# Kernel tuning notes

Hardware: AMD Instinct MI355X
Metric: run time of the kernel (lower is better)

## Reference

```python
import jax, jax.numpy as jnp
import numpy as np

B, S, HID, NH, HD, INTER, NB = 4, 4096, 2048, 32, 64, 8192, 8
EPS = 1e-5
MEM_EPS = 1e-6


def rmsnorm(x, w, eps=EPS):
    return x * jax.lax.rsqrt(jnp.mean(x * x, axis=-1, keepdims=True) + eps) * w


def hbit_linear(x, w):
    # BitNet b1.58: ternary weights (absmean scale) + int8 per-token activation quant (STE).
    ws = jnp.mean(jnp.abs(w)) + 1e-8
    wq = jnp.round(jnp.clip(w / ws, -1.0, 1.0)) * ws
    w_eff = w + jax.lax.stop_gradient(wq - w)
    xs = 127.0 / jnp.clip(jnp.max(jnp.abs(x), axis=-1, keepdims=True), 1e-5, None)
    xq = jnp.clip(jnp.round(x * xs), -128.0, 127.0) / xs
    x_eff = x + jax.lax.stop_gradient(xq - x)
    return x_eff @ w_eff.T


def infini_attention(xn, wq, wk, wv, wo, beta):
    # xn: [B,S,HID]; segment-wise causal local attention + compressive linear memory.
    def proj(w):
        return (xn @ w.T).reshape(B, S, NH, HD).transpose(0, 2, 1, 3)  # [B,H,S,D]

    q, k, v = proj(wq), proj(wk), proj(wv)
    seg = S // NB

    def to_segs(t):
        return t.reshape(B, NH, NB, seg, HD).transpose(2, 0, 1, 3, 4)  # [NB,B,H,seg,D]

    qs, ks, vs = to_segs(q), to_segs(k), to_segs(v)
    mask = jnp.tril(jnp.ones((seg, seg), bool))
    g = jax.nn.sigmoid(beta)[None, :, None, None]  # per-head memory/local mix
    scale = 1.0 / np.sqrt(HD)

    def step(carry, inp):
        M, z = carry  # M:[B,H,D,D], z:[B,H,D]
        qc, kc, vc = inp
        sq = jax.nn.elu(qc) + 1.0
        sk = jax.nn.elu(kc) + 1.0
        a_mem = jnp.einsum('bhsd,bhde->bhse', sq, M) / (
            jnp.einsum('bhsd,bhd->bhs', sq, z)[..., None] + MEM_EPS)
        scores = jnp.einsum('bhqd,bhkd->bhqk', qc, kc) * scale
        scores = jnp.where(mask, scores, -1e9)
        a_loc = jnp.einsum('bhqk,bhkd->bhqd', jax.nn.softmax(scores, axis=-1), vc)
        M = M + jnp.einsum('bhsd,bhse->bhde', sk, vc)
        z = z + sk.sum(axis=2)
        out = g * a_mem + (1.0 - g) * a_loc
        return (M, z), out

    M0 = jnp.zeros((B, NH, HD, HD), xn.dtype)
    z0 = jnp.zeros((B, NH, HD), xn.dtype)
    _, outs = jax.lax.scan(step, (M0, z0), (qs, ks, vs))  # [NB,B,H,seg,D]
    out = outs.transpose(1, 2, 0, 3, 4).reshape(B, NH, S, HD)
    out = out.transpose(0, 2, 1, 3).reshape(B, S, HID)
    return out @ wo.T


def setup_inputs() -> dict:
    key = jax.random.key(0)
    ks = jax.random.split(key, 12)
    std = 0.02
    return {
        'x': jax.random.normal(ks[0], (B, S, HID), jnp.float32),
        'wq': jax.random.normal(ks[1], (HID, HID), jnp.float32) * std,
        'wk': jax.random.normal(ks[2], (HID, HID), jnp.float32) * std,
        'wv': jax.random.normal(ks[3], (HID, HID), jnp.float32) * std,
        'wo': jax.random.normal(ks[4], (HID, HID), jnp.float32) * std,
        'beta': jnp.zeros((NH,), jnp.float32),
        'gate': jnp.zeros((1,), jnp.float32),
        'attn_norm_w': jnp.ones((HID,), jnp.float32),
        'mlp_norm_w': jnp.ones((HID,), jnp.float32),
        'attn_res_norm_w': jnp.ones((HID,), jnp.float32),
        'attn_res_scale': jnp.full((1,), 0.1, jnp.float32),
        'mlp_res_norm_w': jnp.ones((HID,), jnp.float32),
        'mlp_res_scale': jnp.full((1,), 0.1, jnp.float32),
        'ffn_up_w': jax.random.normal(ks[5], (2 * INTER, HID), jnp.float32) * std,
        'ffn_down_w': jax.random.normal(ks[6], (HID, INTER), jnp.float32) * std,
    }


def reference(x, wq, wk, wv, wo, beta, gate, attn_norm_w, mlp_norm_w,
              attn_res_norm_w, attn_res_scale, mlp_res_norm_w, mlp_res_scale,
              ffn_up_w, ffn_down_w):
    residual = x
    xn = rmsnorm(x, attn_norm_w)
    infini_out = infini_attention(xn, wq, wk, wv, wo, beta)
    gated = jax.nn.sigmoid(gate) * infini_out
    x = residual + attn_res_scale * rmsnorm(gated, attn_res_norm_w)
    residual = x
    xn = rmsnorm(x, mlp_norm_w)
    up = hbit_linear(xn, ffn_up_w)
    gate_up, value = jnp.split(up, 2, axis=-1)
    mlp_out = hbit_linear(jax.nn.silu(gate_up) * value, ffn_down_w)
    x = residual + mlp_res_scale * rmsnorm(mlp_out, mlp_res_norm_w)
    return x
```

## Files before the change

kernel.cpp:

```cpp
#include <hip/hip_runtime.h>
#include <cstdint>
#include <cstddef>

typedef unsigned int u32;
typedef unsigned short u16;
typedef __bf16 bf16x8 __attribute__((ext_vector_type(8)));
typedef float f32x4 __attribute__((ext_vector_type(4)));
typedef float f32x16 __attribute__((ext_vector_type(16)));
typedef int i32x4 __attribute__((ext_vector_type(4)));

#define DEV static __device__ __forceinline__

DEV float bf2f(u16 u) { u32 x = ((u32)u) << 16; return __builtin_bit_cast(float, x); }
DEV u16 f2bf(float f) {
  u32 u = __builtin_bit_cast(u32, f);
  u32 r = (u + 0x7fffu + ((u >> 16) & 1u)) >> 16;
  return (u16)r;
}
DEV u32 pkbf(float a, float b) {
  __bf16 ba = (__bf16)a, bb = (__bf16)b;
  return (u32)__builtin_bit_cast(u16, ba) | ((u32)__builtin_bit_cast(u16, bb) << 16);
}
DEV u32 pk4i8(float a, float b, float c, float d) {
  return (u32)(unsigned char)(char)a | ((u32)(unsigned char)(char)b << 8) |
         ((u32)(unsigned char)(char)c << 16) | ((u32)(unsigned char)(char)d << 24);
}
DEV void bf8tof(const uint4 v, float* f) {
  f[0] = bf2f((u16)(v.x & 0xffffu)); f[1] = bf2f((u16)(v.x >> 16));
  f[2] = bf2f((u16)(v.y & 0xffffu)); f[3] = bf2f((u16)(v.y >> 16));
  f[4] = bf2f((u16)(v.z & 0xffffu)); f[5] = bf2f((u16)(v.z >> 16));
  f[6] = bf2f((u16)(v.w & 0xffffu)); f[7] = bf2f((u16)(v.w >> 16));
}
DEV uint4 f8tobf(const float* f) {
  uint4 r;
  r.x = (u32)f2bf(f[0]) | ((u32)f2bf(f[1]) << 16);
  r.y = (u32)f2bf(f[2]) | ((u32)f2bf(f[3]) << 16);
  r.z = (u32)f2bf(f[4]) | ((u32)f2bf(f[5]) << 16);
  r.w = (u32)f2bf(f[6]) | ((u32)f2bf(f[7]) << 16);
  return r;
}
DEV float sigmoidf_(float x) { return 1.f / (1.f + expf(-x)); }

DEV float wred_sum(float v) {
  #pragma unroll
  for (int m = 32; m; m >>= 1) v += __shfl_xor(v, m, 64);
  return v;
}
DEV float wred_max(float v) {
  #pragma unroll
  for (int m = 32; m; m >>= 1) v = fmaxf(v, __shfl_xor(v, m, 64));
  return v;
}
DEV float block_sum(float v, float* red, int nw) {
  v = wred_sum(v);
  int w = threadIdx.x >> 6, l = threadIdx.x & 63;
  if (l == 0) red[w] = v;
  __syncthreads();
  float t = red[0];
  for (int i = 1; i < nw; ++i) t += red[i];
  __syncthreads();
  return t;
}
DEV float block_max(float v, float* red, int nw) {
  v = wred_max(v);
  int w = threadIdx.x >> 6, l = threadIdx.x & 63;
  if (l == 0) red[w] = v;
  __syncthreads();
  float t = red[0];
  for (int i = 1; i < nw; ++i) t = fmaxf(t, red[i]);
  __syncthreads();
  return t;
}
DEV void gload16(const void* g, void* l) {
  __builtin_amdgcn_global_load_lds((const __attribute__((address_space(1))) void*)g,
                                   (__attribute__((address_space(3))) void*)l, 16, 0, 0);
}
DEV bf16x8 ldfrag(const u16* p) {
  uint4 u = *(const uint4*)p;
  return __builtin_bit_cast(bf16x8, u);
}

#define BN_ 4
#define S_ 4096
#define HID_ 2048
#define NH_ 32
#define HD_ 64
#define INTER_ 8192
#define NBSEG_ 8
#define SEG_ 512
#define TOK_ 16384
#define CHROWS_ 4096
#define LDQ_ 6144

__global__ __launch_bounds__(256) void castf2b(const float* __restrict__ a, u16* __restrict__ o) {
  size_t idx = ((size_t)blockIdx.x * 256 + threadIdx.x) * 4;
  float4 v = *(const float4*)(a + idx);
  float f[4] = {v.x, v.y, v.z, v.w};
  uint2 r;
  r.x = (u32)f2bf(f[0]) | ((u32)f2bf(f[1]) << 16);
  r.y = (u32)f2bf(f[2]) | ((u32)f2bf(f[3]) << 16);
  *(uint2*)(o + idx) = r;
}

__global__ __launch_bounds__(256) void absmean_part(const float* __restrict__ w, float* __restrict__ part) {
  __shared__ float red[4];
  size_t base = (size_t)blockIdx.x * 16384 + threadIdx.x * 4;
  float s = 0.f;
  #pragma unroll
  for (int i = 0; i < 16; ++i) {
    float4 v = *(const float4*)(w + base + (size_t)i * 1024);
    s += fabsf(v.x) + fabsf(v.y) + fabsf(v.z) + fabsf(v.w);
  }
  float t = block_sum(s, red, 4);
  if (threadIdx.x == 0) part[blockIdx.x] = t;
}

__global__ __launch_bounds__(256) void absmean_fin(const float* __restrict__ part, int n, float invN, float* __restrict__ outp) {
  __shared__ float red[4];
  float s = 0.f;
  for (int i = threadIdx.x; i < n; i += 256) s += part[i];
  float t = block_sum(s, red, 4);
  if (threadIdx.x == 0) outp[0] = t * invN + 1e-8f;
}

__global__ __launch_bounds__(256) void ternarize_i8(const float* __restrict__ w, const float* __restrict__ wsp, char* __restrict__ o) {
  size_t idx = ((size_t)blockIdx.x * 256 + threadIdx.x) * 4;
  const float inv = 1.f / wsp[0];
  float4 v = *(const float4*)(w + idx);
  float q0 = rintf(fminf(fmaxf(v.x * inv, -1.f), 1.f));
  float q1 = rintf(fminf(fmaxf(v.y * inv, -1.f), 1.f));
  float q2 = rintf(fminf(fmaxf(v.z * inv, -1.f), 1.f));
  float q3 = rintf(fminf(fmaxf(v.w * inv, -1.f), 1.f));
  *(u32*)(o + idx) = pk4i8(q0, q1, q2, q3);
}

__global__ __launch_bounds__(256) void rmsnorm_cast(const float* __restrict__ x, const float* __restrict__ wn, u16* __restrict__ o) {
  __shared__ float red[4];
  const int r = blockIdx.x, tid = threadIdx.x;
  const float* xr = x + (size_t)r * HID_;
  float vx[8];
  #pragma unroll
  for (int i = 0; i < 2; ++i) {
    float4 t = *(const float4*)(xr + tid * 8 + i * 4);
    vx[i * 4 + 0] = t.x; vx[i * 4 + 1] = t.y; vx[i * 4 + 2] = t.z; vx[i * 4 + 3] = t.w;
  }
  float ss = 0.f;
  #pragma unroll
  for (int j = 0; j < 8; ++j) ss += vx[j] * vx[j];
  float tot = block_sum(ss, red, 4);
  float rstd = rsqrtf(tot * (1.f / HID_) + 1e-5f);
  float wv[8];
  #pragma unroll
  for (int i = 0; i < 2; ++i) {
    float4 t = *(const float4*)(wn + tid * 8 + i * 4);
    wv[i * 4 + 0] = t.x; wv[i * 4 + 1] = t.y; wv[i * 4 + 2] = t.z; wv[i * 4 + 3] = t.w;
  }
  float ov[8];
  #pragma unroll
  for (int j = 0; j < 8; ++j) ov[j] = vx[j] * rstd * wv[j];
  *(uint4*)(o + (size_t)r * HID_ + tid * 8) = f8tobf(ov);
}

__global__ __launch_bounds__(256) void resid1_rms2(const float* __restrict__ x, const u16* __restrict__ ao,
    const float* __restrict__ gatep, const float* __restrict__ w1, const float* __restrict__ rsp,
    const float* __restrict__ w2, float* __restrict__ x2, char* __restrict__ xq, float* __restrict__ xs1) {
  __shared__ float red[4];
  const int r = blockIdx.x, tid = threadIdx.x;
  const float g = sigmoidf_(gatep[0]);
  const float rs = rsp[0];
  uint4 av = *(const uint4*)(ao + (size_t)r * HID_ + tid * 8);
  float f[8]; bf8tof(av, f);
  float ss = 0.f;
  #pragma unroll
  for (int j = 0; j < 8; ++j) { f[j] *= g; ss += f[j] * f[j]; }
  float tot = block_sum(ss, red, 4);
  float rstd1 = rsqrtf(tot * (1.f / HID_) + 1e-5f);
  const float* xr = x + (size_t)r * HID_;
  float xv2[8];
  #pragma unroll
  for (int i = 0; i < 2; ++i) {
    float4 xv = *(const float4*)(xr + tid * 8 + i * 4);
    float4 wv = *(const float4*)(w1 + tid * 8 + i * 4);
    xv2[i * 4 + 0] = xv.x + rs * f[i * 4 + 0] * rstd1 * wv.x;
    xv2[i * 4 + 1] = xv.y + rs * f[i * 4 + 1] * rstd1 * wv.y;
    xv2[i * 4 + 2] = xv.z + rs * f[i * 4 + 2] * rstd1 * wv.z;
    xv2[i * 4 + 3] = xv.w + rs * f[i * 4 + 3] * rstd1 * wv.w;
  }
  float* o = x2 + (size_t)r * HID_;
  *(float4*)(o + tid * 8) = float4{xv2[0], xv2[1], xv2[2], xv2[3]};
  *(float4*)(o + tid * 8 + 4) = float4{xv2[4], xv2[5], xv2[6], xv2[7]};
  float ss2 = 0.f;
  #pragma unroll
  for (int j = 0; j < 8; ++j) ss2 += xv2[j] * xv2[j];
  float tot2 = block_sum(ss2, red, 4);
  float rstd2 = rsqrtf(tot2 * (1.f / HID_) + 1e-5f);
  float xn[8]; float mx = 0.f;
  #pragma unroll
  for (int i = 0; i < 2; ++i) {
    float4 wv = *(const float4*)(w2 + tid * 8 + i * 4);
    xn[i * 4 + 0] = xv2[i * 4 + 0] * rstd2 * wv.x;
    xn[i * 4 + 1] = xv2[i * 4 + 1] * rstd2 * wv.y;
    xn[i * 4 + 2] = xv2[i * 4 + 2] * rstd2 * wv.z;
    xn[i * 4 + 3] = xv2[i * 4 + 3] * rstd2 * wv.w;
  }
  #pragma unroll
  for (int j = 0; j < 8; ++j) mx = fmaxf(mx, fabsf(xn[j]));
  float bm = block_max(mx, red, 4);
  float xs = 127.f / fmaxf(bm, 1e-5f);
  float q[8];
  #pragma unroll
  for (int j = 0; j < 8; ++j) q[j] = fminf(fmaxf(rintf(xn[j] * xs), -128.f), 127.f);
  uint2 pw;
  pw.x = pk4i8(q[0], q[1], q[2], q[3]);
  pw.y = pk4i8(q[4], q[5], q[6], q[7]);
  *(uint2*)(xq + (size_t)r * HID_ + tid * 8) = pw;
  if (tid == 0) xs1[r] = xs;
}

__global__ __launch_bounds__(256) void quant_h_i8(const u16* __restrict__ hb, char* __restrict__ hq, float* __restrict__ xs2) {
  __shared__ float red[4];
  const int r = blockIdx.x, tid = threadIdx.x;
  const u16* hr = hb + (size_t)r * INTER_ + tid * 32;
  float f[32];
  #pragma unroll
  for (int k = 0; k < 4; ++k) {
    uint4 v = *(const uint4*)(hr + k * 8);
    bf8tof(v, &f[k * 8]);
  }
  float mx = 0.f;
  #pragma unroll
  for (int j = 0; j < 32; ++j) mx = fmaxf(mx, fabsf(f[j]));
  float bm = block_max(mx, red, 4);
  float xs = 127.f / fmaxf(bm, 1e-5f);
  u32 pw[8];
  #pragma unroll
  for (int k = 0; k < 8; ++k) {
    float q[4];
    #pragma unroll
    for (int j = 0; j < 4; ++j) q[j] = fminf(fmaxf(rintf(f[k * 4 + j] * xs), -128.f), 127.f);
    pw[k] = pk4i8(q[0], q[1], q[2], q[3]);
  }
  char* oq = hq + (size_t)r * INTER_ + tid * 32;
  *(uint4*)oq = uint4{pw[0], pw[1], pw[2], pw[3]};
  *(uint4*)(oq + 16) = uint4{pw[4], pw[5], pw[6], pw[7]};
  if (tid == 0) xs2[r] = xs;
}

__global__ __launch_bounds__(256) void final_resid(const float* __restrict__ x2, const u16* __restrict__ mlp,
    const float* __restrict__ wn, const float* __restrict__ rsp, float* __restrict__ out) {
  __shared__ float red[4];
  const int r = blockIdx.x, tid = threadIdx.x;
  const float rs = rsp[0];
  uint4 mv = *(const uint4*)(mlp + (size_t)r * HID_ + tid * 8);
  float f[8]; bf8tof(mv, f);
  float ss = 0.f;
  #pragma unroll
  for (int j = 0; j < 8; ++j) ss += f[j] * f[j];
  float tot = block_sum(ss, red, 4);
  float rstd = rsqrtf(tot * (1.f / HID_) + 1e-5f);
  const float* xr = x2 + (size_t)r * HID_;
  float* o = out + (size_t)r * HID_;
  #pragma unroll
  for (int i = 0; i < 2; ++i) {
    float4 xv = *(const float4*)(xr + tid * 8 + i * 4);
    float4 wv = *(const float4*)(wn + tid * 8 + i * 4);
    float4 ov;
    ov.x = xv.x + rs * f[i * 4 + 0] * rstd * wv.x;
    ov.y = xv.y + rs * f[i * 4 + 1] * rstd * wv.y;
    ov.z = xv.z + rs * f[i * 4 + 2] * rstd * wv.z;
    ov.w = xv.w + rs * f[i * 4 + 3] * rstd * wv.w;
    *(float4*)(o + tid * 8 + i * 4) = ov;
  }
}

template<int NBN>
__global__ __launch_bounds__(512, 2)
void gemm_bt2(const u16* __restrict__ A, const u16* __restrict__ Bw, u16* __restrict__ C,
              int K, int ldc) {
  __shared__ __align__(16) u16 As[128 * 64];
  __shared__ __align__(16) u16 Bs[256 * 64];
  const int tid = threadIdx.x;
  const int w = tid >> 6, lane = tid & 63;
  const int l15 = lane & 15, l4 = lane >> 4;
  const int wr = (w >> 2) * 64, wc = (w & 3) * 64;
  int id = blockIdx.x;
  const int cpx = (int)gridDim.x >> 3;
  id = (id & 7) * cpx + (id >> 3);
  const int bm = id / NBN, bn = id % NBN;
  const u16* Ag = A + (size_t)bm * 128 * K;
  const u16* Bg = Bw + (size_t)bn * 256 * K;
  f32x4 acc[4][4] = {};
  for (int kk = 0; kk < K; kk += 64) {
    #pragma unroll
    for (int p = 0; p < 2; ++p) {
      const int idx = tid + p * 512;
      const int row = idx >> 3, slot = idx & 7;
      const int ss = slot ^ (row & 7);
      gload16(Ag + (size_t)row * K + kk + ss * 8, &As[idx * 8]);
    }
    #pragma unroll
    for (int p = 0; p < 4; ++p) {
      const int idx = tid + p * 512;
      const int row = idx >> 3, slot = idx & 7;
      const int ss = slot ^ (row & 7);
      gload16(Bg + (size_t)row * K + kk + ss * 8, &Bs[idx * 8]);
    }
    __syncthreads();
    bf16x8 af[4][2], bb[4][2];
    #pragma unroll
    for (int i = 0; i < 4; ++i) {
      const int ra = wr + i * 16 + l15;
      const int rb = wc + i * 16 + l15;
      #pragma unroll
      for (int k2 = 0; k2 < 2; ++k2) {
        const int g8 = k2 * 4 + l4;
        af[i][k2] = ldfrag(&As[ra * 64 + ((g8 ^ (ra & 7)) * 8)]);
        bb[i][k2] = ldfrag(&Bs[rb * 64 + ((g8 ^ (rb & 7)) * 8)]);
      }
    }
    #pragma unroll
    for (int i = 0; i < 4; ++i)
      #pragma unroll
      for (int j = 0; j < 4; ++j)
        #pragma unroll
        for (int k2 = 0; k2 < 2; ++k2)
          acc[i][j] = __builtin_amdgcn_mfma_f32_16x16x32_bf16(af[i][k2], bb[j][k2], acc[i][j], 0, 0, 0);
    __syncthreads();
  }
  #pragma unroll
  for (int i = 0; i < 4; ++i) {
    #pragma unroll
    for (int r = 0; r < 4; ++r) {
      const int row = bm * 128 + wr + i * 16 + l4 * 4 + r;
      #pragma unroll
      for (int j = 0; j < 4; ++j) {
        const int col = bn * 256 + wc + j * 16 + l15;
        C[(size_t)row * ldc + col] = f2bf(acc[i][j][r]);
      }
    }
  }
}

__global__ __launch_bounds__(512, 2)
void gemm_up_i8(const char* __restrict__ A, const char* __restrict__ Bw, u16* __restrict__ H,
                const float* __restrict__ wsp, const float* __restrict__ xs) {
  const int K = HID_;
  __shared__ __align__(16) char As[128 * 128];
  __shared__ __align__(16) char Gs[128 * 128];
  __shared__ __align__(16) char Vs[128 * 128];
  const int tid = threadIdx.x;
  const int w = tid >> 6, lane = tid & 63;
  const int l15 = lane & 15, l4 = lane >> 4;
  const int wr = (w >> 2) * 64, wc = (w & 3) * 32;
  int id = blockIdx.x;
  const int cpx = (int)gridDim.x >> 3;
  id = (id & 7) * cpx + (id >> 3);
  const int bm = id & 31, bn = id >> 5;
  const char* Ag = A + (size_t)bm * 128 * K;
  const char* Gg = Bw + (size_t)bn * 128 * K;
  const char* Vg = Bw + ((size_t)INTER_ + bn * 128) * K;
  i32x4 ag[4][2] = {}, av[4][2] = {};
  for (int kk = 0; kk < K; kk += 128) {
    #pragma unroll
    for (int p = 0; p < 2; ++p) {
      const int idx = tid + p * 512;
      const int row = idx >> 3, slot = idx & 7;
      const int ss = slot ^ (row & 7);
      gload16(Ag + (size_t)row * K + kk + ss * 16, &As[idx * 16]);
      gload16(Gg + (size_t)row * K + kk + ss * 16, &Gs[idx * 16]);
      gload16(Vg + (size_t)row * K + kk + ss * 16, &Vs[idx * 16]);
    }
    __syncthreads();
    i32x4 af_[4][2], gf_[2][2], vf_[2][2];
    #pragma unroll
    for (int i = 0; i < 4; ++i) {
      const int r = wr + i * 16 + l15;
      #pragma unroll
      for (int k2 = 0; k2 < 2; ++k2) {
        const int j = k2 * 4 + l4;
        af_[i][k2] = *(const i32x4*)&As[r * 128 + ((j ^ (r & 7)) * 16)];
      }
    }
    #pragma unroll
    for (int jj = 0; jj < 2; ++jj) {
      const int r = wc + jj * 16 + l15;
      #pragma unroll
      for (int k2 = 0; k2 < 2; ++k2) {
        const int j = k2 * 4 + l4;
        gf_[jj][k2] = *(const i32x4*)&Gs[r * 128 + ((j ^ (r & 7)) * 16)];
        vf_[jj][k2] = *(const i32x4*)&Vs[r * 128 + ((j ^ (r & 7)) * 16)];
      }
    }
    #pragma unroll
    for (int i = 0; i < 4; ++i)
      #pragma unroll
      for (int jj = 0; jj < 2; ++jj)
        #pragma unroll
        for (int k2 = 0; k2 < 2; ++k2) {
          ag[i][jj] = __builtin_amdgcn_mfma_i32_16x16x64_i8(af_[i][k2], gf_[jj][k2], ag[i][jj], 0, 0, 0);
          av[i][jj] = __builtin_amdgcn_mfma_i32_16x16x64_i8(af_[i][k2], vf_[jj][k2], av[i][jj], 0, 0, 0);
        }
    __syncthreads();
  }
  const float ws0 = wsp[0];
  #pragma unroll
  for (int i = 0; i < 4; ++i) {
    #pragma unroll
    for (int r = 0; r < 4; ++r) {
      const int row = bm * 128 + wr + i * 16 + l4 * 4 + r;
      const float scl = ws0 / xs[row];
      #pragma unroll
      for (int jj = 0; jj < 2; ++jj) {
        const int col = bn * 128 + wc + jj * 16 + l15;
        const float og = (float)ag[i][jj][r] * scl;
        const float ov = (float)av[i][jj][r] * scl;
        const float hv = og * ov / (1.f + expf(-og));
        H[(size_t)row * INTER_ + col] = f2bf(hv);
      }
    }
  }
}

__global__ __launch_bounds__(256, 2)
void gemm_dn_i8(const char* __restrict__ A, const char* __restrict__ Bw, u16* __restrict__ C,
                const float* __restrict__ wsp, const float* __restrict__ xs) {
  const int N = HID_, K = INTER_;
  __shared__ __align__(16) char As[128 * 128];
  __shared__ __align__(16) char Bs[128 * 128];
  const int tid = threadIdx.x;
  const int wv = tid >> 6, lane = tid & 63;
  const int l15 = lane & 15, l4 = lane >> 4;
  const int wr = (wv >> 1) * 64, wc = (wv & 1) * 64;
  const int bm = blockIdx.y, bn = blockIdx.x;
  const char* Ag = A + (size_t)bm * 128 * K;
  const char* Bg = Bw + (size_t)bn * 128 * K;
  i32x4 acc[4][4] = {};
  for (int kk = 0; kk < K; kk += 128) {
    #pragma unroll
    for (int p = 0; p < 4; ++p) {
      const int idx = tid + p * 256;
      const int row = idx >> 3, slot = idx & 7;
      const int ss = slot ^ (row & 7);
      gload16(Ag + (size_t)row * K + kk + ss * 16, &As[idx * 16]);
      gload16(Bg + (size_t)row * K + kk + ss * 16, &Bs[idx * 16]);
    }
    __syncthreads();
    i32x4 af_[4][2], bb_[4][2];
    #pragma unroll
    for (int i = 0; i < 4; ++i) {
      const int ra = wr + i * 16 + l15;
      const int rb = wc + i * 16 + l15;
      #pragma unroll
      for (int k2 = 0; k2 < 2; ++k2) {
        const int j = k2 * 4 + l4;
        af_[i][k2] = *(const i32x4*)&As[ra * 128 + ((j ^ (ra & 7)) * 16)];
        bb_[i][k2] = *(const i32x4*)&Bs[rb * 128 + ((j ^ (rb & 7)) * 16)];
      }
    }
    #pragma unroll
    for (int i = 0; i < 4; ++i)
      #pragma unroll
      for (int j = 0; j < 4; ++j)
        #pragma unroll
        for (int k2 = 0; k2 < 2; ++k2)
          acc[i][j] = __builtin_amdgcn_mfma_i32_16x16x64_i8(af_[i][k2], bb_[j][k2], acc[i][j], 0, 0, 0);
    __syncthreads();
  }
  const float ws0 = wsp[0];
  #pragma unroll
  for (int i = 0; i < 4; ++i) {
    #pragma unroll
    for (int r = 0; r < 4; ++r) {
      const int row = bm * 128 + wr + i * 16 + l4 * 4 + r;
      const float scl = ws0 / xs[row];
      #pragma unroll
      for (int j = 0; j < 4; ++j) {
        const int col = bn * 128 + wc + j * 16 + l15;
        C[(size_t)row * N + col] = f2bf((float)acc[i][j][r] * scl);
      }
    }
  }
}

DEV void write_otile(const f32x16 oc, float invl, char* stgB, u16* alocrow,
                     int da, int l31, int hi, int lane) {
  #pragma unroll
  for (int r = 0; r < 16; ++r) {
    const int dl = (r & 3) + 8 * (r >> 2) + 4 * hi;
    *(u16*)(stgB + l31 * 64 + ((dl * 2) ^ ((l31 & 3) << 4))) = f2bf(oc[r] * invl);
  }
  #pragma unroll
  for (int p = 0; p < 2; ++p) {
    const int s = lane >> 1;
    const int d8 = (lane & 1) * 8 + p * 16;
    const uint4 val = *(const uint4*)(stgB + s * 64 + ((d8 * 2) ^ ((s & 3) << 4)));
    *(uint4*)(alocrow + (size_t)s * HD_ + da * 32 + d8) = val;
  }
}

__global__ __launch_bounds__(512)
void attn_local_mfma(const u16* __restrict__ q, const u16* __restrict__ k, const u16* __restrict__ v,
                     u16* __restrict__ aloc, float* __restrict__ Useg, float* __restrict__ yseg, int ldq) {
  __shared__ __align__(16) u16 Ks[512 * 64];
  __shared__ __align__(16) u16 VT[64 * 512];
  __shared__ __align__(16) u16 SP[9216];
  const int bid = blockIdx.x;
  const int c = bid >> 7, bh = bid & 127;
  const int b = bh >> 5, h = bh & 31;
  const int tid = threadIdx.x, w = tid >> 6, lane = tid & 63;
  const int l31 = lane & 31, hi = lane >> 5;
  const size_t rowbase = ((size_t)b * S_ + c * SEG_) * (size_t)ldq + h * HD_;
  const u16* qg = q + rowbase;
  const u16* kg = k + rowbase;
  const u16* vg = v + rowbase;
  char* KsB = (char*)Ks;
  char* VTB = (char*)VT;
  #pragma unroll
  for (int p = 0; p < 8; ++p) {
    const int idx = tid + p * 512;
    const int t = idx >> 3, dg = idx & 7;
    gload16(kg + (size_t)t * ldq + (size_t)((dg ^ (t & 7)) * 8), KsB + idx * 16);
  }
  #pragma unroll
  for (int u = 0; u < 2; ++u) {
    const int unit = tid + u * 512;
    const int g2 = unit & 127, dg = unit >> 7;
    const uint4 r0 = *(const uint4*)(vg + (size_t)(4 * g2 + 0) * ldq + dg * 8);
    const uint4 r1 = *(const uint4*)(vg + (size_t)(4 * g2 + 1) * ldq + dg * 8);
    const uint4 r2 = *(const uint4*)(vg + (size_t)(4 * g2 + 2) * ldq + dg * 8);
    const uint4 r3 = *(const uint4*)(vg + (size_t)(4 * g2 + 3) * ldq + dg * 8);
    const u16* e0 = (const u16*)&r0;
    const u16* e1 = (const u16*)&r1;
    const u16* e2 = (const u16*)&r2;
    const u16* e3 = (const u16*)&r3;
    #pragma unroll
    for (int j = 0; j < 8; ++j) {
      const int d = dg * 8 + j;
      uint2 wv2;
      wv2.x = (u32)e0[j] | ((u32)e1[j] << 16);
      wv2.y = (u32)e2[j] | ((u32)e3[j] << 16);
      *(uint2*)(VTB + d * 1024 + ((8 * g2) ^ ((d & 7) << 4))) = wv2;
    }
  }
  uint4 qf[2][4];
  #pragma unroll
  for (int qi = 0; qi < 2; ++qi) {
    const int qt = qi == 0 ? w : 15 - w;
    #pragma unroll
    for (int ks = 0; ks < 4; ++ks)
      qf[qi][ks] = *(const uint4*)(qg + (size_t)(qt * 32 + l31) * ldq + ks * 16 + hi * 8);
  }
  __syncthreads();

  const size_t arow = (size_t)(b * NH_ + h) * S_ + c * SEG_;
  const int swzk = (l31 & 7) << 4;
  char* stgB = (char*)SP + w * 2048;
  #pragma unroll
  for (int qi = 0; qi < 2; ++qi) {
    const int qt = qi == 0 ? w : 15 - w;
    f32x16 o0 = {}, o1 = {};
    float m = -3e38f, l = 0.f;
    const int nb = qt + 1;
    for (int tb = 0; tb < nb; ++tb) {
      f32x16 st = {};
      #pragma unroll
      for (int ks = 0; ks < 4; ++ks) {
        const uint4 ka = *(const uint4*)(KsB + (tb * 32 + l31) * 128 + (((ks * 16 + hi * 8) * 2) ^ swzk));
        st = __builtin_amdgcn_mfma_f32_32x32x16_bf16(__builtin_bit_cast(bf16x8, ka),
                                                     __builtin_bit_cast(bf16x8, qf[qi][ks]), st, 0, 0, 0);
      }
      if (tb == nb - 1) {
        #pragma unroll
        for (int r = 0; r < 16; ++r) {
          const int tl = (r & 3) + 8 * (r >> 2) + 4 * hi;
          if (tl > l31) st[r] = -3e38f;
        }
      }
      float tm = st[0];
      #pragma unroll
      for (int r = 1; r < 16; ++r) tm = fmaxf(tm, st[r]);
      tm = fmaxf(tm, __shfl_xor(tm, 32, 64));
      const float mn = fmaxf(m, tm);
      const float fac = __expf((m - mn) * 0.125f);
      float pr[16]; float ps = 0.f;
      #pragma unroll
      for (int r = 0; r < 16; ++r) { pr[r] = __expf((st[r] - mn) * 0.125f); ps += pr[r]; }
      ps += __shfl_xor(ps, 32, 64);
      l = l * fac + ps;
      m = mn;
      #pragma unroll
      for (int r = 0; r < 16; ++r) { o0[r] *= fac; o1[r] *= fac; }
      #pragma unroll
      for (int c2 = 0; c2 < 2; ++c2) {
        const int bi = c2 * 8;
        const u32 a0 = pkbf(pr[bi + 0], pr[bi + 1]);
        const u32 a1 = pkbf(pr[bi + 2], pr[bi + 3]);
        const u32 a2 = pkbf(pr[bi + 4], pr[bi + 5]);
        const u32 a3 = pkbf(pr[bi + 6], pr[bi + 7]);
        const u32 x0 = (u32)__shfl_xor((int)a0, 32, 64);
        const u32 x1 = (u32)__shfl_xor((int)a1, 32, 64);
        const u32 x2 = (u32)__shfl_xor((int)a2, 32, 64);
        const u32 x3 = (u32)__shfl_xor((int)a3, 32, 64);
        uint4 pw;
        pw.x = hi ? x2 : a0;
        pw.y = hi ? x3 : a1;
        pw.z = hi ? a2 : x0;
        pw.w = hi ? a3 : x1;
        const bf16x8 pfr = __builtin_bit_cast(bf16x8, pw);
        const int tO = (tb * 32 + c2 * 16 + hi * 8) * 2;
        const uint4 v0 = *(const uint4*)(VTB + l31 * 1024 + (tO ^ swzk));
        const uint4 v1 = *(const uint4*)(VTB + (32 + l31) * 1024 + (tO ^ swzk));
        o0 = __builtin_amdgcn_mfma_f32_32x32x16_bf16(__builtin_bit_cast(bf16x8, v0), pfr, o0, 0, 0, 0);
        o1 = __builtin_amdgcn_mfma_f32_32x32x16_bf16(__builtin_bit_cast(bf16x8, v1), pfr, o1, 0, 0, 0);
      }
    }
    const float invl = 1.f / l;
    u16* alocrow = aloc + (arow + qt * 32) * HD_;
    write_otile(o0, invl, stgB, alocrow, 0, l31, hi, lane);
    write_otile(o1, invl, stgB, alocrow, 1, l31, hi, lane);
  }

  __syncthreads();
  float* Ured = (float*)SP;
  float* yred = (float*)((char*)SP + 16384);
  for (int i = tid; i < 4096; i += 512) Ured[i] = 0.f;
  yred[tid] = 0.f;
  __syncthreads();
  f32x16 u00 = {}, u01 = {}, u10 = {}, u11 = {};
  float y0 = 0.f, y1 = 0.f;
  #pragma unroll
  for (int kc = 0; kc < 4; ++kc) {
    const int t0 = w * 64 + kc * 16 + hi * 8;
    uint4 af[2];
    #pragma unroll
    for (int da2 = 0; da2 < 2; ++da2) {
      const int d = da2 * 32 + l31;
      u32 wds[4];
      #pragma unroll
      for (int jp = 0; jp < 4; ++jp) {
        const int ta = t0 + jp * 2;
        const int tb2 = ta + 1;
        const float kfa = bf2f(*(const u16*)(KsB + ta * 128 + ((d * 2) ^ ((ta & 7) << 4))));
        const float kfb = bf2f(*(const u16*)(KsB + tb2 * 128 + ((d * 2) ^ ((tb2 & 7) << 4))));
        const float sa = kfa > 0.f ? kfa + 1.f : __expf(kfa);
        const float sb = kfb > 0.f ? kfb + 1.f : __expf(kfb);
        if (da2 == 0) y0 += sa + sb; else y1 += sa + sb;
        wds[jp] = pkbf(sa, sb);
      }
      af[da2].x = wds[0]; af[da2].y = wds[1]; af[da2].z = wds[2]; af[da2].w = wds[3];
    }
    const int tO = t0 * 2;
    const uint4 vb0 = *(const uint4*)(VTB + l31 * 1024 + (tO ^ swzk));
    const uint4 vb1 = *(const uint4*)(VTB + (32 + l31) * 1024 + (tO ^ swzk));
    const bf16x8 a0f = __builtin_bit_cast(bf16x8, af[0]);
    const bf16x8 a1f = __builtin_bit_cast(bf16x8, af[1]);
    const bf16x8 b0f = __builtin_bit_cast(bf16x8, vb0);
    const bf16x8 b1f = __builtin_bit_cast(bf16x8, vb1);
    u00 = __builtin_amdgcn_mfma_f32_32x32x16_bf16(a0f, b0f, u00, 0, 0, 0);
    u01 = __builtin_amdgcn_mfma_f32_32x32x16_bf16(a0f, b1f, u01, 0, 0, 0);
    u10 = __builtin_amdgcn_mfma_f32_32x32x16_bf16(a1f, b0f, u10, 0, 0, 0);
    u11 = __builtin_amdgcn_mfma_f32_32x32x16_bf16(a1f, b1f, u11, 0, 0, 0);
  }
  y0 += __shfl_xor(y0, 32, 64);
  y1 += __shfl_xor(y1, 32, 64);
  if (hi == 0) { yred[w * 64 + l31] = y0; yred[w * 64 + 32 + l31] = y1; }
  for (int ww = 0; ww < 8; ++ww) {
    if (w == ww) {
      #pragma unroll
      for (int r = 0; r < 16; ++r) {
        const int dl = (r & 3) + 8 * (r >> 2) + 4 * hi;
        Ured[dl * 64 + l31]            += u00[r];
        Ured[dl * 64 + 32 + l31]       += u01[r];
        Ured[(32 + dl) * 64 + l31]     += u10[r];
        Ured[(32 + dl) * 64 + 32 + l31]+= u11[r];
      }
    }
    __syncthreads();
  }
  float* Ug = Useg + (size_t)(c * 128 + bh) * 4096;
  for (int i = tid; i < 4096; i += 512) Ug[i] = Ured[i];
  if (tid < 64) {
    float a2 = 0.f;
    #pragma unroll
    for (int ww = 0; ww < 8; ++ww) a2 += yred[ww * 64 + tid];
    yseg[(size_t)(c * 128 + bh) * 64 + tid] = a2;
  }
}

__global__ __launch_bounds__(256)
void attn_prefix(const float* __restrict__ Useg, const float* __restrict__ yseg,
                 float* __restrict__ Mpre, float* __restrict__ zpre) {
  const int bh = blockIdx.x, tid = threadIdx.x;
  for (int idx = tid; idx < 4096; idx += 256) {
    float a2 = 0.f;
    #pragma unroll
    for (int c = 0; c < 8; ++c) {
      const size_t o = ((size_t)(c * 128 + bh)) * 4096 + idx;
      Mpre[o] = a2;
      a2 += Useg[o];
    }
  }
  if (tid < 64) {
    float a2 = 0.f;
    #pragma unroll
    for (int c = 0; c < 8; ++c) {
      const size_t o = ((size_t)(c * 128 + bh)) * 64 + tid;
      zpre[o] = a2;
      a2 += yseg[o];
    }
  }
}

__global__ __launch_bounds__(512)
void attn_combine(const u16* __restrict__ q, const u16* __restrict__ aloc,
                  const float* __restrict__ Mpre, const float* __restrict__ zpre,
                  const float* __restrict__ beta, u16* __restrict__ attno, int ldq) {
  __shared__ __align__(16) u16 MbT[64 * 64];
  __shared__ float z_lds[64];
  __shared__ float amem[8][16 * 65];
  const int bid = blockIdx.x;
  const int c = bid >> 7, bh = bid & 127;
  const int b = bh >> 5, h = bh & 31;
  const int tid = threadIdx.x, w = tid >> 6, lane = tid & 63;
  const int l15 = lane & 15, l4 = lane >> 4;
  const size_t pre = (size_t)(c * 128 + bh);
  char* MbB = (char*)MbT;
  for (int i = tid; i < 4096; i += 512) {
    const int d = i >> 6, e = i & 63;
    *(u16*)(MbB + (((e * 64 + d) * 2) ^ ((e & 7) << 4))) = f2bf(Mpre[pre * 4096 + i]);
  }
  if (tid < 64) z_lds[tid] = zpre[pre * 64 + tid];
  __syncthreads();
  bf16x8 bb[2][4];
  #pragma unroll
  for (int ks = 0; ks < 2; ++ks)
    #pragma unroll
    for (int jt = 0; jt < 4; ++jt) {
      const int e = jt * 16 + l15;
      const uint4 u = *(const uint4*)(MbB + (((e * 64 + ks * 32 + l4 * 8) * 2) ^ ((e & 7) << 4)));
      bb[ks][jt] = __builtin_bit_cast(bf16x8, u);
    }
  const float g = sigmoidf_(beta[h]);
  const float og = 1.f - g;
  const u16* qg = q + ((size_t)b * S_ + c * SEG_) * ldq + h * HD_;
  const size_t arow = (size_t)(b * NH_ + h) * S_ + c * SEG_;
  u16* orow = attno + ((size_t)b * S_ + c * SEG_) * HID_ + h * HD_;
  const int rr = lane >> 2, cq = (lane & 3) * 16;
  #pragma unroll
  for (int mi = 0; mi < 4; ++mi) {
    const int s0 = w * 64 + mi * 16;
    f32x4 acc[4] = {};
    float pd = 0.f;
    #pragma unroll
    for (int ks = 0; ks < 2; ++ks) {
      const uint4 qv = *(const uint4*)(qg + (size_t)(s0 + l15) * ldq + ks * 32 + l4 * 8);
      float f[8]; bf8tof(qv, f);
      float sq[8];
      #pragma unroll
      for (int j = 0; j < 8; ++j) {
        sq[j] = f[j] > 0.f ? f[j] + 1.f : __expf(f[j]);
        pd = fmaf(sq[j], z_lds[ks * 32 + l4 * 8 + j], pd);
      }
      uint4 pw;
      pw.x = pkbf(sq[0], sq[1]); pw.y = pkbf(sq[2], sq[3]);
      pw.z = pkbf(sq[4], sq[5]); pw.w = pkbf(sq[6], sq[7]);
      const bf16x8 af = __builtin_bit_cast(bf16x8, pw);
      #pragma unroll
      for (int jt = 0; jt < 4; ++jt)
        acc[jt] = __builtin_amdgcn_mfma_f32_16x16x32_bf16(af, bb[ks][jt], acc[jt], 0, 0, 0);
    }
    pd += __shfl_xor(pd, 16, 64);
    pd += __shfl_xor(pd, 32, 64);
    pd += 1e-6f;
    float dinv[4];
    #pragma unroll
    for (int r = 0; r < 4; ++r) dinv[r] = 1.f / __shfl(pd, l4 * 4 + r, 64);
    #pragma unroll
    for (int jt = 0; jt < 4; ++jt)
      #pragma unroll
      for (int r = 0; r < 4; ++r)
        amem[w][(l4 * 4 + r) * 65 + jt * 16 + l15] = acc[jt][r] * dinv[r];
    const int s = s0 + rr;
    const u16* alr = aloc + (arow + s) * HD_ + cq;
    const uint4 a0 = *(const uint4*)alr;
    const uint4 a1 = *(const uint4*)(alr + 8);
    float alf[16];
    bf8tof(a0, alf); bf8tof(a1, alf + 8);
    float ov[16];
    #pragma unroll
    for (int t = 0; t < 16; ++t)
      ov[t] = g * amem[w][rr * 65 + cq + t] + og * alf[t];
    *(uint4*)(orow + (size_t)s * HID_ + cq) = f8tobf(ov);
    *(uint4*)(orow + (size_t)s * HID_ + cq + 8) = f8tobf(ov + 8);
  }
}

extern "C" void kernel_launch(void* const* d_in, const int* in_sizes, int n_in,
                              void* d_out, int out_size, void* d_ws, size_t ws_size,
                              hipStream_t stream) {
  const float* x    = (const float*)d_in[0];
  const float* wq   = (const float*)d_in[1];
  const float* wk   = (const float*)d_in[2];
  const float* wv   = (const float*)d_in[3];
  const float* wo   = (const float*)d_in[4];
  const float* beta = (const float*)d_in[5];
  const float* gate = (const float*)d_in[6];
  const float* anw  = (const float*)d_in[7];
  const float* mnw  = (const float*)d_in[8];
  const float* arnw = (const float*)d_in[9];
  const float* arsc = (const float*)d_in[10];
  const float* mrnw = (const float*)d_in[11];
  const float* mrsc = (const float*)d_in[12];
  const float* fup  = (const float*)d_in[13];
  const float* fdn  = (const float*)d_in[14];

  char* W = (char*)d_ws;
  const size_t MB = 1ull << 20;
  u16*   xn1   = (u16*)(W + 0);
  u16*   attno = (u16*)(W + 0);
  u16*   mlpb  = (u16*)(W + 0);
  u16*   qkv   = (u16*)(W + 64 * MB);
  char*  xq1   = (char*)(W + 64 * MB);
  u16*   aob   = (u16*)(W + 128 * MB);
  u16*   hbuf  = (u16*)(W + 128 * MB);
  u16*   alocb = (u16*)(W + 256 * MB);
  float* x2    = (float*)(W + 192 * MB);
  float* Useg  = (float*)(W + 320 * MB);
  float* Mpre  = (float*)(W + 336 * MB);
  float* yseg  = (float*)(W + 352 * MB);
  float* zpre  = (float*)(W + 352 * MB + 262144);
  float* xs1   = (float*)(W + 352 * MB + 524288);
  float* xs2   = (float*)(W + 352 * MB + 589824);
  float* wsu   = (float*)(W + 352 * MB + 655360);
  float* wsd   = (float*)(W + 352 * MB + 655616);
  float* partU = (float*)(W + 352 * MB + 655872);
  float* partD = (float*)(W + 352 * MB + 664064);
  u16*   w16qkv= (u16*)(W + 353 * MB);
  u16*   w16o  = (u16*)(W + 377 * MB);
  char*  wqup  = (char*)(W + 385 * MB);
  char*  wqdn  = (char*)(W + 417 * MB);
  char*  hq    = (char*)(W + 433 * MB);

  castf2b<<<4096, 256, 0, stream>>>(wq, w16qkv);
  castf2b<<<4096, 256, 0, stream>>>(wk, w16qkv + (size_t)HID_ * HID_);
  castf2b<<<4096, 256, 0, stream>>>(wv, w16qkv + 2 * (size_t)HID_ * HID_);
  castf2b<<<4096, 256, 0, stream>>>(wo, w16o);
  absmean_part<<<2048, 256, 0, stream>>>(fup, partU);
  absmean_part<<<1024, 256, 0, stream>>>(fdn, partD);
  absmean_fin<<<1, 256, 0, stream>>>(partU, 2048, 1.f / 33554432.f, wsu);
  absmean_fin<<<1, 256, 0, stream>>>(partD, 1024, 1.f / 16777216.f, wsd);
  ternarize_i8<<<32768, 256, 0, stream>>>(fup, wsu, wqup);
  ternarize_i8<<<16384, 256, 0, stream>>>(fdn, wsd, wqdn);

  rmsnorm_cast<<<16384, 256, 0, stream>>>(x, anw, xn1);
  gemm_bt2<24><<<3072, 512, 0, stream>>>(xn1, w16qkv, qkv, HID_, LDQ_);
  attn_local_mfma<<<1024, 512, 0, stream>>>(qkv, qkv + HID_, qkv + 2 * HID_, alocb, Useg, yseg, LDQ_);
  attn_prefix<<<128, 256, 0, stream>>>(Useg, yseg, Mpre, zpre);
  attn_combine<<<1024, 512, 0, stream>>>(qkv, alocb, Mpre, zpre, beta, attno, LDQ_);
  gemm_bt2<8><<<1024, 512, 0, stream>>>(attno, w16o, aob, HID_, HID_);
  resid1_rms2<<<16384, 256, 0, stream>>>(x, aob, gate, arnw, arsc, mnw, x2, xq1, xs1);

  for (int cc = 0; cc < 4; ++cc) {
    const size_t base = (size_t)cc * CHROWS_;
    gemm_up_i8<<<2048, 512, 0, stream>>>(xq1 + base * HID_, wqup, hbuf, wsu, xs1 + base);
    quant_h_i8<<<4096, 256, 0, stream>>>(hbuf, hq, xs2 + base);
    gemm_dn_i8<<<dim3(16, 32), 256, 0, stream>>>(hq, wqdn, mlpb + base * HID_, wsd, xs2 + base);
  }
  final_resid<<<16384, 256, 0, stream>>>(x2, mlpb, mrnw, mrsc, (float*)d_out);
}
```

Measured before the change: 1.970 ms.

## Triple-buffer LDS tiles in bf16 GEMM with async prefetch two tiles ahead

Replaces the load-sync-compute-sync loop of the bf16 GEMM with a three-stage LDS ring buffer. Global-to-LDS loads for tile t+2 are issued before computing tile t, and completion is tracked with explicit vmcnt waits and a single barrier per iteration. The goal is to hide global memory latency behind MFMA work and remove one barrier per K step. The cost is about 144KB of LDS per block, which likely allows only one 512-thread block per CU instead of the two the launch bounds target, cutting occupancy.

```diff
diff --git a/kernel.cpp b/kernel.cpp
--- a/kernel.cpp
+++ b/kernel.cpp
@@ -277,8 +277,8 @@
 __global__ __launch_bounds__(512, 2)
 void gemm_bt2(const u16* __restrict__ A, const u16* __restrict__ Bw, u16* __restrict__ C,
               int K, int ldc) {
-  __shared__ __align__(16) u16 As[128 * 64];
-  __shared__ __align__(16) u16 Bs[256 * 64];
+  __shared__ __align__(16) u16 As[3][128 * 64];
+  __shared__ __align__(16) u16 Bs[3][256 * 64];
   const int tid = threadIdx.x;
   const int w = tid >> 6, lane = tid & 63;
   const int l15 = lane & 15, l4 = lane >> 4;
@@ -289,23 +289,40 @@
   const int bm = id / NBN, bn = id % NBN;
   const u16* Ag = A + (size_t)bm * 128 * K;
   const u16* Bg = Bw + (size_t)bn * 256 * K;
+  const int nt = K >> 6;
+  const int ra0 = tid >> 3, sa0 = ((tid & 7) ^ (ra0 & 7)) * 8;
+  const int ra1 = (tid + 512) >> 3, sa1 = (((tid + 512) & 7) ^ (ra1 & 7)) * 8;
+
   f32x4 acc[4][4] = {};
-  for (int kk = 0; kk < K; kk += 64) {
-    #pragma unroll
-    for (int p = 0; p < 2; ++p) {
-      const int idx = tid + p * 512;
-      const int row = idx >> 3, slot = idx & 7;
-      const int ss = slot ^ (row & 7);
-      gload16(Ag + (size_t)row * K + kk + ss * 8, &As[idx * 8]);
-    }
+  #pragma unroll
+  for (int tt = 0; tt < 2; ++tt) {
+    const int kk = tt << 6;
+    gload16(Ag + (size_t)ra0 * K + kk + sa0, &As[tt][tid * 8]);
+    gload16(Ag + (size_t)ra1 * K + kk + sa1, &As[tt][(tid + 512) * 8]);
     #pragma unroll
     for (int p = 0; p < 4; ++p) {
       const int idx = tid + p * 512;
-      const int row = idx >> 3, slot = idx & 7;
-      const int ss = slot ^ (row & 7);
-      gload16(Bg + (size_t)row * K + kk + ss * 8, &Bs[idx * 8]);
-    }
-    __syncthreads();
+      const int row = idx >> 3, ss = ((idx & 7) ^ (row & 7)) * 8;
+      gload16(Bg + (size_t)row * K + kk + ss, &Bs[tt][idx * 8]);
+    }
+  }
+  asm volatile("s_waitcnt vmcnt(6)" ::: "memory");
+  asm volatile("s_barrier" ::: "memory");
+
+  int cur = 0;
+  for (int t = 0; t < nt; ++t) {
+    if (t + 2 < nt) {
+      int b2 = cur + 2; if (b2 >= 3) b2 -= 3;
+      const int kk = (t + 2) << 6;
+      gload16(Ag + (size_t)ra0 * K + kk + sa0, &As[b2][tid * 8]);
+      gload16(Ag + (size_t)ra1 * K + kk + sa1, &As[b2][(tid + 512) * 8]);
+      #pragma unroll
+      for (int p = 0; p < 4; ++p) {
+        const int idx = tid + p * 512;
+        const int row = idx >> 3, ss = ((idx & 7) ^ (row & 7)) * 8;
+        gload16(Bg + (size_t)row * K + kk + ss, &Bs[b2][idx * 8]);
+      }
+    }
     bf16x8 af[4][2], bb[4][2];
     #pragma unroll
     for (int i = 0; i < 4; ++i) {
@@ -314,8 +331,8 @@
       #pragma unroll
       for (int k2 = 0; k2 < 2; ++k2) {
         const int g8 = k2 * 4 + l4;
-        af[i][k2] = ldfrag(&As[ra * 64 + ((g8 ^ (ra & 7)) * 8)]);
-        bb[i][k2] = ldfrag(&Bs[rb * 64 + ((g8 ^ (rb & 7)) * 8)]);
+        af[i][k2] = ldfrag(&As[cur][ra * 64 + ((g8 ^ (ra & 7)) * 8)]);
+        bb[i][k2] = ldfrag(&Bs[cur][rb * 64 + ((g8 ^ (rb & 7)) * 8)]);
       }
     }
     #pragma unroll
@@ -325,7 +342,12 @@
         #pragma unroll
         for (int k2 = 0; k2 < 2; ++k2)
           acc[i][j] = __builtin_amdgcn_mfma_f32_16x16x32_bf16(af[i][k2], bb[j][k2], acc[i][j], 0, 0, 0);
-    __syncthreads();
+    if (t + 1 < nt) {
+      if (t + 2 < nt) asm volatile("s_waitcnt vmcnt(6)" ::: "memory");
+      else            asm volatile("s_waitcnt vmcnt(0)" ::: "memory");
+      asm volatile("s_barrier" ::: "memory");
+    }
+    ++cur; if (cur >= 3) cur = 0;
   }
   #pragma unroll
   for (int i = 0; i < 4; ++i) {
```

After: 2.206 ms. 12.0% more time.
